# Kernel optimization log

Measured on AMD Instinct MI355X. Metric: run time of the kernel, lower is better.

The kernel has to match this reference:

```python
import jax, jax.numpy as jnp
import numpy as np

DT = 1.0          # integration timestep (ms)
SIGMA = 0.5       # gauss_std for surrogate (unused in pure fwd spike)
AMPLITUDE = 0.3   # dampening_factor
N = 50000         # neurons
R = 4             # receptor types
D = 5             # max_delay
E = 5000000       # recurrent synapses
B = 4             # batch


def setup_inputs() -> dict:
    key = jax.random.key(0)
    ks = jax.random.split(key, 20)
    f = jnp.float32
    inputs = jax.random.normal(ks[0], (B, N * R), f) * 0.1
    # z_buf holds binary spikes for the last D steps
    z_buf = jax.random.bernoulli(ks[1], 0.05, (B, N * D)).astype(f)
    v = jax.random.uniform(ks[2], (B, N), f, 0.0, 1.0)
    r = jnp.zeros((B, N), f)
    asc_1 = jax.random.normal(ks[3], (B, N), f)
    asc_2 = jax.random.normal(ks[4], (B, N), f)
    psc_rise = jax.random.normal(ks[5], (B, N * R), f) * 0.5
    psc = jax.random.normal(ks[6], (B, N * R), f)
    rec_w = jax.random.normal(ks[7], (E,), f) * 0.01
    rec_rows = jax.random.randint(ks[8], (E,), 0, N * R, jnp.int32)
    rec_cols = jax.random.randint(ks[9], (E,), 0, N * D, jnp.int32)
    syn_decay = jax.random.uniform(ks[10], (N, R), f, 0.5, 0.99)
    psc_initial = jax.random.uniform(ks[11], (N, R), f, 0.1, 1.0)
    t_ref = jax.random.uniform(ks[12], (N,), f, 1.0, 4.0)
    asc_amps = jax.random.normal(ks[13], (N, 2), f)
    k = jax.random.normal(ks[14], (N, 2), f)  # inv-sigmoid space, read via sigmoid
    v_th = jnp.ones((N,), f)
    e_l = jnp.zeros((N,), f)
    v_reset = jnp.zeros((N,), f)
    g = jax.random.uniform(ks[15], (N,), f, 0.1, 1.0)
    decay = jax.random.uniform(ks[16], (N,), f, 0.8, 0.99)
    current_factor = jax.random.uniform(ks[17], (N,), f, 0.1, 1.0)
    voltage_scale = jnp.ones((N,), f) * 20.0
    voltage_offset = jnp.ones((N,), f) * -70.0
    return dict(inputs=inputs, z_buf=z_buf, v=v, r=r, asc_1=asc_1, asc_2=asc_2,
                psc_rise=psc_rise, psc=psc, rec_w=rec_w, rec_rows=rec_rows,
                rec_cols=rec_cols, syn_decay=syn_decay, psc_initial=psc_initial,
                t_ref=t_ref, asc_amps=asc_amps, k=k, v_th=v_th, e_l=e_l,
                v_reset=v_reset, g=g, decay=decay, current_factor=current_factor,
                voltage_scale=voltage_scale, voltage_offset=voltage_offset)


def _step(inputs, z_buf, v, r, asc_1, asc_2, psc_rise, psc,
          rec_w, rec_rows, rec_cols, syn_decay, psc_initial, t_ref,
          asc_amps, k, v_th, e_l, v_reset, g, decay, current_factor,
          voltage_scale, voltage_offset):
    shaped_z_buf = z_buf.reshape(B, D, N)
    prev_z = shaped_z_buf[:, 0]                      # most recent spikes [B,N]
    psc_rise_r = psc_rise.reshape(B, N, R)
    psc_r = psc.reshape(B, N, R)

    # sparse recurrent matmul: W[N*R, N*D] @ z_buf^T -> [N*R, B]
    vals = rec_w[:, None] * z_buf.T[rec_cols]        # [E, B] gather
    i_rec = jax.ops.segment_sum(vals, rec_rows, num_segments=N * R).T  # [B, N*R]

    rec_inputs = (i_rec + inputs).reshape(B, N, R)
    new_psc_rise = syn_decay * psc_rise_r + rec_inputs * psc_initial
    new_psc = psc_r * syn_decay + DT * syn_decay * psc_rise_r

    new_r = jax.nn.relu(r + prev_z * t_ref - DT)

    kk = jax.nn.sigmoid(k)                           # param_k_read()
    new_asc_1 = jnp.exp(-DT * kk[:, 0]) * asc_1 + prev_z * asc_amps[:, 0]
    new_asc_2 = jnp.exp(-DT * kk[:, 1]) * asc_2 + prev_z * asc_amps[:, 1]

    reset_current = prev_z * (v_reset - v_th)
    input_current = psc_r.sum(-1)                    # old psc
    c1 = input_current + asc_1 + asc_2 + g * e_l
    new_v = decay * v + current_factor * c1 + reset_current

    v_sc = (new_v - v_th) / (v_th - e_l)
    new_z = (v_sc > 0.0).astype(v_sc.dtype)          # spike_gauss forward
    new_z = jnp.where(new_r > 0.0, jnp.zeros_like(new_z), new_z)

    new_z_buf = jnp.concatenate([new_z[:, None], shaped_z_buf[:, :-1]], axis=1)
    out_v = new_v * voltage_scale + voltage_offset
    return (new_z, out_v, new_r, new_asc_1, new_asc_2,
            new_psc_rise.reshape(B, N * R), new_psc.reshape(B, N * R),
            new_z_buf.reshape(B, N * D))


def reference(inputs, z_buf, v, r, asc_1, asc_2, psc_rise, psc,
              rec_w, rec_rows, rec_cols, syn_decay, psc_initial, t_ref,
              asc_amps, k, v_th, e_l, v_reset, g, decay, current_factor,
              voltage_scale, voltage_offset):
    outs = _step(inputs, z_buf, v, r, asc_1, asc_2, psc_rise, psc,
                 rec_w, rec_rows, rec_cols, syn_decay, psc_initial, t_ref,
                 asc_amps, k, v_th, e_l, v_reset, g, decay, current_factor,
                 voltage_scale, voltage_offset)
    # pack outputs + new state into one [B, N*(5+2R+D)] array
    return jnp.concatenate(outs, axis=-1)
```

## Files before the change

kernel.cpp:

```cpp
#include <hip/hip_runtime.h>

#define Nn 50000
#define Rr 4
#define Dd 5
#define Ee 5000000
#define Bb 4
#define NRr (Nn * Rr)
#define NDd (Nn * Dd)
#define OUT_STRIDE (18 * Nn)

typedef int   v4i __attribute__((ext_vector_type(4)));
typedef float v4f __attribute__((ext_vector_type(4)));

struct P {
    const float* inputs; const float* z_buf; const float* v; const float* r;
    const float* asc1; const float* asc2; const float* psc_rise; const float* psc;
    const float* rec_w; const int* rec_rows; const int* rec_cols;
    const float* syn_decay; const float* psc_initial; const float* t_ref;
    const float* asc_amps; const float* k; const float* v_th; const float* e_l;
    const float* v_reset; const float* g; const float* decay;
    const float* current_factor; const float* vscale; const float* voffset;
    float* out; float* i_rec; unsigned char* z_pack;
};

__global__ __launch_bounds__(256) void pack_neuron_kernel(P p) {
    int i = blockIdx.x * 256 + threadIdx.x;

    if (i < Bb * NRr / 4)
        ((float4*)p.i_rec)[i] = make_float4(0.f, 0.f, 0.f, 0.f);

    if (i < NDd) {
        unsigned m = 0;
#pragma unroll
        for (int b = 0; b < Bb; ++b)
            if (p.z_buf[(size_t)b * NDd + i] != 0.0f) m |= (1u << b);
        p.z_pack[i] = (unsigned char)m;
    }

    if (i < Bb * Nn) {
        int b = i / Nn;
        int n = i - b * Nn;
        const size_t bn  = (size_t)b * Nn + n;
        const size_t bnr = (size_t)b * NRr + (size_t)n * 4;

        float prev_z = p.z_buf[(size_t)b * NDd + n];
        float4 pr = *(const float4*)(p.psc_rise + bnr);
        float4 pc = *(const float4*)(p.psc + bnr);
        float4 sd = *(const float4*)(p.syn_decay + (size_t)n * 4);

        float4 npc;
        npc.x = pc.x * sd.x + sd.x * pr.x;
        npc.y = pc.y * sd.y + sd.y * pr.y;
        npc.z = pc.z * sd.z + sd.z * pr.z;
        npc.w = pc.w * sd.w + sd.w * pr.w;
        float input_current = pc.x + pc.y + pc.z + pc.w;

        float new_r = fmaxf(p.r[bn] + prev_z * p.t_ref[n] - 1.0f, 0.0f);

        float2 kv = *(const float2*)(p.k + (size_t)n * 2);
        float2 aa = *(const float2*)(p.asc_amps + (size_t)n * 2);
        float kk0 = 1.0f / (1.0f + expf(-kv.x));
        float kk1 = 1.0f / (1.0f + expf(-kv.y));
        float a1 = p.asc1[bn];
        float a2 = p.asc2[bn];
        float na1 = expf(-kk0) * a1 + prev_z * aa.x;
        float na2 = expf(-kk1) * a2 + prev_z * aa.y;

        float vth = p.v_th[n];
        float el  = p.e_l[n];
        float reset_current = prev_z * (p.v_reset[n] - vth);
        float c1 = input_current + a1 + a2 + p.g[n] * el;
        float new_v = p.decay[n] * p.v[bn] + p.current_factor[n] * c1
                      + reset_current;
        float v_sc = (new_v - vth) / (vth - el);
        float new_z = (v_sc > 0.0f) ? 1.0f : 0.0f;
        if (new_r > 0.0f) new_z = 0.0f;
        float out_v = new_v * p.vscale[n] + p.voffset[n];

        float* ob = p.out + (size_t)b * OUT_STRIDE;
        ob[n]          = new_z;
        ob[Nn + n]     = out_v;
        ob[2 * Nn + n] = new_r;
        ob[3 * Nn + n] = na1;
        ob[4 * Nn + n] = na2;
        *(float4*)(ob + 9 * Nn + (size_t)n * 4) = npc;
        ob[13 * Nn + n] = new_z;
#pragma unroll
        for (int d = 0; d < Dd - 1; ++d)
            ob[14 * Nn + (size_t)d * Nn + n] =
                p.z_buf[(size_t)b * NDd + (size_t)d * Nn + n];
    }
}

__global__ __launch_bounds__(256) void edge_kernel(P p) {
    int tid = blockIdx.x * 256 + threadIdx.x;
    if (tid >= Ee / 4) return;

    v4i c = __builtin_nontemporal_load(&((const v4i*)p.rec_cols)[tid]);
    unsigned m0 = p.z_pack[c.x];
    unsigned m1 = p.z_pack[c.y];
    unsigned m2 = p.z_pack[c.z];
    unsigned m3 = p.z_pack[c.w];
    if (!(m0 | m1 | m2 | m3)) return;

    v4i rw = __builtin_nontemporal_load(&((const v4i*)p.rec_rows)[tid]);
    v4f w  = __builtin_nontemporal_load(&((const v4f*)p.rec_w)[tid]);
    float* i_rec = p.i_rec;
    auto do_edge = [&](unsigned mm, int row, float wv) {
        if (mm & 1u) atomicAdd(&i_rec[0 * NRr + row], wv);
        if (mm & 2u) atomicAdd(&i_rec[1 * NRr + row], wv);
        if (mm & 4u) atomicAdd(&i_rec[2 * NRr + row], wv);
        if (mm & 8u) atomicAdd(&i_rec[3 * NRr + row], wv);
    };
    do_edge(m0, rw.x, w.x);
    do_edge(m1, rw.y, w.y);
    do_edge(m2, rw.z, w.z);
    do_edge(m3, rw.w, w.w);
}

__global__ __launch_bounds__(256) void psc_rise_kernel(P p) {
    int tid = blockIdx.x * 256 + threadIdx.x;
    if (tid >= Bb * Nn) return;
    int b = tid / Nn;
    int n = tid - b * Nn;
    const size_t bnr = (size_t)b * NRr + (size_t)n * 4;
    float4 ir  = *(const float4*)(p.i_rec + bnr);
    float4 in4 = *(const float4*)(p.inputs + bnr);
    float4 pr  = *(const float4*)(p.psc_rise + bnr);
    float4 sd  = *(const float4*)(p.syn_decay + (size_t)n * 4);
    float4 pi  = *(const float4*)(p.psc_initial + (size_t)n * 4);
    float4 npr;
    npr.x = sd.x * pr.x + (ir.x + in4.x) * pi.x;
    npr.y = sd.y * pr.y + (ir.y + in4.y) * pi.y;
    npr.z = sd.z * pr.z + (ir.z + in4.z) * pi.z;
    npr.w = sd.w * pr.w + (ir.w + in4.w) * pi.w;
    float* ob = p.out + (size_t)b * OUT_STRIDE;
    *(float4*)(ob + 5 * Nn + (size_t)n * 4) = npr;
}

extern "C" void kernel_launch(void* const* d_in, const int* in_sizes, int n_in,
                              void* d_out, int out_size, void* d_ws, size_t ws_size,
                              hipStream_t stream) {
    P p;
    p.inputs        = (const float*)d_in[0];
    p.z_buf         = (const float*)d_in[1];
    p.v             = (const float*)d_in[2];
    p.r             = (const float*)d_in[3];
    p.asc1          = (const float*)d_in[4];
    p.asc2          = (const float*)d_in[5];
    p.psc_rise      = (const float*)d_in[6];
    p.psc           = (const float*)d_in[7];
    p.rec_w         = (const float*)d_in[8];
    p.rec_rows      = (const int*)d_in[9];
    p.rec_cols      = (const int*)d_in[10];
    p.syn_decay     = (const float*)d_in[11];
    p.psc_initial   = (const float*)d_in[12];
    p.t_ref         = (const float*)d_in[13];
    p.asc_amps      = (const float*)d_in[14];
    p.k             = (const float*)d_in[15];
    p.v_th          = (const float*)d_in[16];
    p.e_l           = (const float*)d_in[17];
    p.v_reset       = (const float*)d_in[18];
    p.g             = (const float*)d_in[19];
    p.decay         = (const float*)d_in[20];
    p.current_factor= (const float*)d_in[21];
    p.vscale        = (const float*)d_in[22];
    p.voffset       = (const float*)d_in[23];
    p.out           = (float*)d_out;

    p.i_rec  = (float*)d_ws;
    p.z_pack = (unsigned char*)d_ws + 3200000;

    pack_neuron_kernel<<<(NDd + 255) / 256, 256, 0, stream>>>(p);
    edge_kernel<<<(Ee / 4 + 255) / 256, 256, 0, stream>>>(p);
    psc_rise_kernel<<<(Bb * Nn + 255) / 256, 256, 0, stream>>>(p);
}
```

Before: 208.6 us.

## Privatize recurrent current accumulators per XCC with workgroup-scope atomics

The edge scatter now accumulates into one private copy of the recurrent-current buffer per XCC, chosen by reading the hardware XCC id. It uses relaxed workgroup-scope atomics instead of device-scope atomicAdd, and a reduction kernel then sums the 8 copies before computing psc_rise. The aim is to keep the atomic traffic inside each XCC's L2 rather than paying cross-die coherent atomics. In exchange it zeroes and reads eight times more workspace, and relies on workgroup-scope atomics behaving coherently across CUs within one XCC. If the workspace is too small it falls back to a two-pass half-row variant or to the original device-atomic path.

```diff
diff --git a/kernel.cpp b/kernel.cpp
--- a/kernel.cpp
+++ b/kernel.cpp
@@ -8,6 +8,10 @@
 #define NRr (Nn * Rr)
 #define NDd (Nn * Dd)
 #define OUT_STRIDE (18 * Nn)
+#define CFULL (Bb * NRr)
+#define HROWS (NRr / 2)
+#define CHALF (Bb * HROWS)
+#define NHALF (Nn / 2)
 
 typedef int   v4i __attribute__((ext_vector_type(4)));
 typedef float v4f __attribute__((ext_vector_type(4)));
@@ -20,14 +24,22 @@
     const float* asc_amps; const float* k; const float* v_th; const float* e_l;
     const float* v_reset; const float* g; const float* decay;
     const float* current_factor; const float* vscale; const float* voffset;
-    float* out; float* i_rec; unsigned char* z_pack;
+    float* out; float* copies; unsigned char* z_pack;
+    int nzero4;
 };
+
+__device__ __forceinline__ unsigned my_xcc() {
+    unsigned xcc;
+    asm volatile("s_getreg_b32 %0, hwreg(HW_REG_XCC_ID)" : "=s"(xcc));
+    return xcc & 7u;
+}
 
 __global__ __launch_bounds__(256) void pack_neuron_kernel(P p) {
     int i = blockIdx.x * 256 + threadIdx.x;
-
-    if (i < Bb * NRr / 4)
-        ((float4*)p.i_rec)[i] = make_float4(0.f, 0.f, 0.f, 0.f);
+    int nthreads = gridDim.x * 256;
+
+    for (int t = i; t < p.nzero4; t += nthreads)
+        ((float4*)p.copies)[t] = make_float4(0.f, 0.f, 0.f, 0.f);
 
     if (i < NDd) {
         unsigned m = 0;
@@ -92,20 +104,136 @@
     }
 }
 
-__global__ __launch_bounds__(256) void edge_kernel(P p) {
+__global__ __launch_bounds__(256) void edge_priv8(P p) {
     int tid = blockIdx.x * 256 + threadIdx.x;
     if (tid >= Ee / 4) return;
-
-    v4i c = __builtin_nontemporal_load(&((const v4i*)p.rec_cols)[tid]);
+    float* my = p.copies + (size_t)my_xcc() * CFULL;
+
+    v4i c = ((const v4i*)p.rec_cols)[tid];
     unsigned m0 = p.z_pack[c.x];
     unsigned m1 = p.z_pack[c.y];
     unsigned m2 = p.z_pack[c.z];
     unsigned m3 = p.z_pack[c.w];
     if (!(m0 | m1 | m2 | m3)) return;
-
-    v4i rw = __builtin_nontemporal_load(&((const v4i*)p.rec_rows)[tid]);
-    v4f w  = __builtin_nontemporal_load(&((const v4f*)p.rec_w)[tid]);
-    float* i_rec = p.i_rec;
+    v4i rw = ((const v4i*)p.rec_rows)[tid];
+    v4f w  = ((const v4f*)p.rec_w)[tid];
+    auto acc = [&](int idx, float wv) {
+        __hip_atomic_fetch_add(&my[idx], wv, __ATOMIC_RELAXED,
+                               __HIP_MEMORY_SCOPE_WORKGROUP);
+    };
+    auto do_edge = [&](unsigned mm, int row, float wv) {
+        if (mm & 1u) acc(0 * NRr + row, wv);
+        if (mm & 2u) acc(1 * NRr + row, wv);
+        if (mm & 4u) acc(2 * NRr + row, wv);
+        if (mm & 8u) acc(3 * NRr + row, wv);
+    };
+    do_edge(m0, rw.x, w.x);
+    do_edge(m1, rw.y, w.y);
+    do_edge(m2, rw.z, w.z);
+    do_edge(m3, rw.w, w.w);
+}
+
+__global__ __launch_bounds__(256) void reduce8(P p) {
+    int tid = blockIdx.x * 256 + threadIdx.x;
+    if (tid >= Bb * Nn) return;
+    int b = tid / Nn;
+    int n = tid - b * Nn;
+    const size_t bnr = (size_t)b * NRr + (size_t)n * 4;
+    float4 s = make_float4(0.f, 0.f, 0.f, 0.f);
+#pragma unroll
+    for (int cp = 0; cp < 8; ++cp) {
+        float4 t = *(const float4*)(p.copies + (size_t)cp * CFULL + bnr);
+        s.x += t.x; s.y += t.y; s.z += t.z; s.w += t.w;
+    }
+    float4 in4 = *(const float4*)(p.inputs + bnr);
+    float4 pr  = *(const float4*)(p.psc_rise + bnr);
+    float4 sd  = *(const float4*)(p.syn_decay + (size_t)n * 4);
+    float4 pi  = *(const float4*)(p.psc_initial + (size_t)n * 4);
+    float4 npr;
+    npr.x = sd.x * pr.x + (s.x + in4.x) * pi.x;
+    npr.y = sd.y * pr.y + (s.y + in4.y) * pi.y;
+    npr.z = sd.z * pr.z + (s.z + in4.z) * pi.z;
+    npr.w = sd.w * pr.w + (s.w + in4.w) * pi.w;
+    float* ob = p.out + (size_t)b * OUT_STRIDE;
+    *(float4*)(ob + 5 * Nn + (size_t)n * 4) = npr;
+}
+
+__global__ __launch_bounds__(256) void edge_priv8_half(P p, int pass) {
+    int tid = blockIdx.x * 256 + threadIdx.x;
+    if (tid >= Ee / 4) return;
+    float* my = p.copies + (size_t)my_xcc() * CHALF;
+    const int base = pass * HROWS;
+
+    v4i rw = ((const v4i*)p.rec_rows)[tid];
+    unsigned r0 = (unsigned)(rw.x - base);
+    unsigned r1 = (unsigned)(rw.y - base);
+    unsigned r2 = (unsigned)(rw.z - base);
+    unsigned r3 = (unsigned)(rw.w - base);
+    bool a0 = r0 < HROWS, a1 = r1 < HROWS, a2 = r2 < HROWS, a3 = r3 < HROWS;
+    if (!(a0 | a1 | a2 | a3)) return;
+
+    v4i c = ((const v4i*)p.rec_cols)[tid];
+    unsigned m0 = a0 ? p.z_pack[c.x] : 0u;
+    unsigned m1 = a1 ? p.z_pack[c.y] : 0u;
+    unsigned m2 = a2 ? p.z_pack[c.z] : 0u;
+    unsigned m3 = a3 ? p.z_pack[c.w] : 0u;
+    if (!(m0 | m1 | m2 | m3)) return;
+    v4f w = ((const v4f*)p.rec_w)[tid];
+    auto acc = [&](int idx, float wv) {
+        __hip_atomic_fetch_add(&my[idx], wv, __ATOMIC_RELAXED,
+                               __HIP_MEMORY_SCOPE_WORKGROUP);
+    };
+    auto do_edge = [&](unsigned mm, unsigned rr, float wv) {
+        if (mm & 1u) acc(0 * HROWS + (int)rr, wv);
+        if (mm & 2u) acc(1 * HROWS + (int)rr, wv);
+        if (mm & 4u) acc(2 * HROWS + (int)rr, wv);
+        if (mm & 8u) acc(3 * HROWS + (int)rr, wv);
+    };
+    do_edge(m0, r0, w.x);
+    do_edge(m1, r1, w.y);
+    do_edge(m2, r2, w.z);
+    do_edge(m3, r3, w.w);
+}
+
+__global__ __launch_bounds__(256) void reduce8_half(P p, int pass) {
+    int tid = blockIdx.x * 256 + threadIdx.x;
+    if (tid >= Bb * NHALF) return;
+    int b = tid / NHALF;
+    int nh = tid - b * NHALF;
+    int n = pass * NHALF + nh;
+    const size_t cof = (size_t)b * HROWS + (size_t)nh * 4;
+    float4 s = make_float4(0.f, 0.f, 0.f, 0.f);
+#pragma unroll
+    for (int cp = 0; cp < 8; ++cp) {
+        float* src = p.copies + (size_t)cp * CHALF + cof;
+        float4 t = *(const float4*)src;
+        s.x += t.x; s.y += t.y; s.z += t.z; s.w += t.w;
+        *(float4*)src = make_float4(0.f, 0.f, 0.f, 0.f);
+    }
+    const size_t bnr = (size_t)b * NRr + (size_t)n * 4;
+    float4 in4 = *(const float4*)(p.inputs + bnr);
+    float4 pr  = *(const float4*)(p.psc_rise + bnr);
+    float4 sd  = *(const float4*)(p.syn_decay + (size_t)n * 4);
+    float4 pi  = *(const float4*)(p.psc_initial + (size_t)n * 4);
+    float4 npr;
+    npr.x = sd.x * pr.x + (s.x + in4.x) * pi.x;
+    npr.y = sd.y * pr.y + (s.y + in4.y) * pi.y;
+    npr.z = sd.z * pr.z + (s.z + in4.z) * pi.z;
+    npr.w = sd.w * pr.w + (s.w + in4.w) * pi.w;
+    float* ob = p.out + (size_t)b * OUT_STRIDE;
+    *(float4*)(ob + 5 * Nn + (size_t)n * 4) = npr;
+}
+
+__global__ __launch_bounds__(256) void edge_dev(P p) {
+    int tid = blockIdx.x * 256 + threadIdx.x;
+    if (tid >= Ee / 4) return;
+    v4i c = ((const v4i*)p.rec_cols)[tid];
+    unsigned m0 = p.z_pack[c.x], m1 = p.z_pack[c.y];
+    unsigned m2 = p.z_pack[c.z], m3 = p.z_pack[c.w];
+    if (!(m0 | m1 | m2 | m3)) return;
+    v4i rw = ((const v4i*)p.rec_rows)[tid];
+    v4f w  = ((const v4f*)p.rec_w)[tid];
+    float* i_rec = p.copies;
     auto do_edge = [&](unsigned mm, int row, float wv) {
         if (mm & 1u) atomicAdd(&i_rec[0 * NRr + row], wv);
         if (mm & 2u) atomicAdd(&i_rec[1 * NRr + row], wv);
@@ -118,13 +246,13 @@
     do_edge(m3, rw.w, w.w);
 }
 
-__global__ __launch_bounds__(256) void psc_rise_kernel(P p) {
+__global__ __launch_bounds__(256) void psc_rise_dev(P p) {
     int tid = blockIdx.x * 256 + threadIdx.x;
     if (tid >= Bb * Nn) return;
     int b = tid / Nn;
     int n = tid - b * Nn;
     const size_t bnr = (size_t)b * NRr + (size_t)n * 4;
-    float4 ir  = *(const float4*)(p.i_rec + bnr);
+    float4 ir  = *(const float4*)(p.copies + bnr);
     float4 in4 = *(const float4*)(p.inputs + bnr);
     float4 pr  = *(const float4*)(p.psc_rise + bnr);
     float4 sd  = *(const float4*)(p.syn_decay + (size_t)n * 4);
@@ -159,8 +287,8 @@
     p.asc_amps      = (const float*)d_in[14];
     p.k             = (const float*)d_in[15];
     p.v_th          = (const float*)d_in[16];
+    p.v_reset       = (const float*)d_in[18];
     p.e_l           = (const float*)d_in[17];
-    p.v_reset       = (const float*)d_in[18];
     p.g             = (const float*)d_in[19];
     p.decay         = (const float*)d_in[20];
     p.current_factor= (const float*)d_in[21];
@@ -168,10 +296,32 @@
     p.voffset       = (const float*)d_in[23];
     p.out           = (float*)d_out;
 
-    p.i_rec  = (float*)d_ws;
-    p.z_pack = (unsigned char*)d_ws + 3200000;
-
-    pack_neuron_kernel<<<(NDd + 255) / 256, 256, 0, stream>>>(p);
-    edge_kernel<<<(Ee / 4 + 255) / 256, 256, 0, stream>>>(p);
-    psc_rise_kernel<<<(Bb * Nn + 255) / 256, 256, 0, stream>>>(p);
-}
+    const size_t needA = (size_t)8 * CFULL * 4 + NDd;
+    const size_t needB = (size_t)8 * CHALF * 4 + NDd;
+    p.copies = (float*)d_ws;
+
+    const int gridK1   = (NDd + 255) / 256;
+    const int gridEdge = (Ee / 4 + 255) / 256;
+
+    if (ws_size >= needA) {
+        p.z_pack = (unsigned char*)d_ws + (size_t)8 * CFULL * 4;
+        p.nzero4 = 8 * CFULL / 4;
+        pack_neuron_kernel<<<gridK1, 256, 0, stream>>>(p);
+        edge_priv8<<<gridEdge, 256, 0, stream>>>(p);
+        reduce8<<<(Bb * Nn + 255) / 256, 256, 0, stream>>>(p);
+    } else if (ws_size >= needB) {
+        p.z_pack = (unsigned char*)d_ws + (size_t)8 * CHALF * 4;
+        p.nzero4 = 8 * CHALF / 4;
+        pack_neuron_kernel<<<gridK1, 256, 0, stream>>>(p);
+        edge_priv8_half<<<gridEdge, 256, 0, stream>>>(p, 0);
+        reduce8_half<<<(Bb * NHALF + 255) / 256, 256, 0, stream>>>(p, 0);
+        edge_priv8_half<<<gridEdge, 256, 0, stream>>>(p, 1);
+        reduce8_half<<<(Bb * NHALF + 255) / 256, 256, 0, stream>>>(p, 1);
+    } else {
+        p.z_pack = (unsigned char*)d_ws + (size_t)CFULL * 4;
+        p.nzero4 = CFULL / 4;
+        pack_neuron_kernel<<<gridK1, 256, 0, stream>>>(p);
+        edge_dev<<<gridEdge, 256, 0, stream>>>(p);
+        psc_rise_dev<<<(Bb * Nn + 255) / 256, 256, 0, stream>>>(p);
+    }
+}
```

Measured after the change: 220.0 us. 5.5% more time.
